# Kernel tuning notes

Measured on AMD Instinct MI355X. Metric: run time of the kernel, lower is better.

The kernel has to match this reference:

```python
import jax, jax.numpy as jnp
import numpy as np


def setup_inputs() -> dict:
    key = jax.random.key(0)
    ks = jax.random.split(key, 6)
    B, H, W, C = 4, 64, 64, 256
    D = 256  # d_model
    s = 0.02
    return {
        "features": jax.random.normal(ks[0], (B, H, W, C), dtype=jnp.float32),
        "Wq": jax.random.normal(ks[1], (C, D), dtype=jnp.float32) * s,
        "bq": jnp.zeros((D,), dtype=jnp.float32),
        "Wk": jax.random.normal(ks[2], (C, D), dtype=jnp.float32) * s,
        "bk": jnp.zeros((D,), dtype=jnp.float32),
        "Wv": jax.random.normal(ks[3], (C, D), dtype=jnp.float32) * s,
        "bv": jnp.zeros((D,), dtype=jnp.float32),
        "Wo": jax.random.normal(ks[4], (D, C), dtype=jnp.float32) * s,
        "bo": jnp.zeros((C,), dtype=jnp.float32),
    }


def reference(features, Wq, bq, Wk, bk, Wv, bv, Wo, bo):
    # features: [B, H, W, C] (NHWC). 1x1 convs are per-pixel GEMMs, so flatten
    # spatial dims to N = H*W tokens and do single-head self-attention.
    B, H, W, C = features.shape
    D = Wq.shape[1]
    x = features.reshape(B, H * W, C)          # [B, N, C]
    q = x @ Wq + bq                            # [B, N, D]
    k = x @ Wk + bk                            # [B, N, D]
    v = x @ Wv + bv                            # [B, N, D]
    scale = np.float32(1.0 / np.sqrt(D))
    scores = jnp.einsum("bnd,bmd->bnm", q, k) * scale   # [B, N, N]
    attn = jax.nn.softmax(scores, axis=-1)               # [B, N, N]
    out = jnp.einsum("bnm,bmd->bnd", attn, v)            # [B, N, D]
    out = out @ Wo + bo                                  # [B, N, C]
    return out.reshape(B, H, W, C)
```

## Files before the change

kernel.cpp:

```cpp
#include <hip/hip_runtime.h>
#include <hip/hip_bf16.h>


typedef __attribute__((ext_vector_type(8))) short short8;
typedef __attribute__((ext_vector_type(4))) short short4v;
typedef __attribute__((ext_vector_type(4))) float floatx4;

#define NB 4
#define NT 4096
#define CD 256
#define MTOT (NB * NT)

__device__ __forceinline__ short bf16s(float f) {
    union { float f; unsigned u; } a; a.f = f;
    unsigned u = a.u;
    return (short)((u + 0x7fffu + ((u >> 16) & 1u)) >> 16);
}

__device__ __forceinline__ float bf2f(short s) {
    union { unsigned u; float f; } a;
    a.u = ((unsigned)(unsigned short)s) << 16;
    return a.f;
}

__device__ __forceinline__ short8 ld8(const short* p) {
    return *(const short8*)p;
}

__device__ __forceinline__ floatx4 mfma16(short8 a, short8 b, floatx4 c) {
    return __builtin_amdgcn_mfma_f32_16x16x32_bf16(a, b, c, 0, 0, 0);
}

__device__ __forceinline__ void dma16(const void* g, void* l) {
    __builtin_amdgcn_global_load_lds(
        (const __attribute__((address_space(1))) void*)g,
        (__attribute__((address_space(3))) void*)l, 16, 0, 0);
}

__global__ __launch_bounds__(256) void k_convx(const float* __restrict__ x,
                                               short* __restrict__ xb) {
    int i = (blockIdx.x * 256 + threadIdx.x) * 4;
    float4 v = *(const float4*)(x + i);
    short4v o;
    o.x = bf16s(v.x); o.y = bf16s(v.y); o.z = bf16s(v.z); o.w = bf16s(v.w);
    *(short4v*)(xb + i) = o;
}

__global__ __launch_bounds__(256) void k_convw(const float* __restrict__ w0,
                                               const float* __restrict__ w1,
                                               const float* __restrict__ w2,
                                               const float* __restrict__ w3,
                                               short* __restrict__ wt) {
    int z = blockIdx.y;
    const float* w = (z == 0) ? w0 : (z == 1) ? w1 : (z == 2) ? w2 : w3;
    int c = blockIdx.x;
    int n = threadIdx.x;
    wt[z * 65536 + n * 256 + c] = bf16s(w[c * 256 + n]);
}

__global__ __launch_bounds__(256) void k_proj3(const short* __restrict__ A,
                                               const short* __restrict__ Wt,
                                               const float* __restrict__ bq,
                                               const float* __restrict__ bk,
                                               const float* __restrict__ bv,
                                               short* __restrict__ Qb,
                                               short* __restrict__ Kb,
                                               short* __restrict__ Vt) {
    __shared__ __align__(16) short Ws[16384];
    int z = blockIdx.z;
    const short* W = Wt + z * 65536;
    const float* bias = (z == 0) ? bq : (z == 1) ? bk : bv;
    float scale = (z == 0) ? 0.0625f : 1.0f;
    int m0 = blockIdx.x * 128;
    int n0 = blockIdx.y * 64;
    int tid = threadIdx.x;
    int w = tid >> 6, l = tid & 63, r = l & 15, q = l >> 4;

#pragma unroll
    for (int cg = 0; cg < 8; ++cg)
        dma16(W + (size_t)(n0 + w * 16 + r) * CD + (cg * 4 + q) * 8,
              &Ws[w * 4096 + cg * 512]);
    __syncthreads();

    const short* a0 = A + (size_t)(m0 + w * 32 + r) * CD;
    const short* a1 = a0 + 16 * CD;
    floatx4 acc[2][4];
#pragma unroll
    for (int rt = 0; rt < 2; ++rt)
#pragma unroll
        for (int j = 0; j < 4; ++j) acc[rt][j] = (floatx4){0.f, 0.f, 0.f, 0.f};
#pragma unroll
    for (int c = 0; c < 8; ++c) {
        short8 af0 = ld8(a0 + c * 32 + q * 8);
        short8 af1 = ld8(a1 + c * 32 + q * 8);
#pragma unroll
        for (int j = 0; j < 4; ++j) {
            short8 wf = ld8(&Ws[j * 4096 + c * 512 + l * 8]);
            acc[0][j] = mfma16(af0, wf, acc[0][j]);
            acc[1][j] = mfma16(af1, wf, acc[1][j]);
        }
    }
#pragma unroll
    for (int rt = 0; rt < 2; ++rt)
#pragma unroll
        for (int j = 0; j < 4; ++j) {
            int col = n0 + j * 16 + r;
            float bvv = bias[col];
#pragma unroll
            for (int i = 0; i < 4; ++i) {
                int row = m0 + w * 32 + rt * 16 + q * 4 + i;
                short s = bf16s((acc[rt][j][i] + bvv) * scale);
                if (z == 0) Qb[(size_t)row * CD + col] = s;
                else if (z == 1) Kb[(size_t)row * CD + col] = s;
                else {
                    int bb = row >> 12, lm = row & (NT - 1);
                    Vt[((size_t)bb * CD + col) * NT + lm] = s;
                }
            }
        }
}

__global__ __launch_bounds__(256, 3) void k_attn(const short* __restrict__ Qb,
                                                 const short* __restrict__ Kb,
                                                 const short* __restrict__ Vt,
                                                 short* __restrict__ Op0,
                                                 short* __restrict__ Op1,
                                                 short* __restrict__ Op2,
                                                 float* __restrict__ Lp,
                                                 int nks) {
    __shared__ __align__(16) short Ks[2][8192];
    __shared__ __align__(16) short P[64][36];

    const int tid = threadIdx.x;
    const int w = tid >> 6;
    const int l = tid & 63;
    const int r = l & 15, q = l >> 4;
    const int b = blockIdx.y;
    const int ks = blockIdx.z;
    const int m0 = blockIdx.x * 64;
    const int qq = 128 / nks, rem = 128 % nks;
    const int u0 = ks * qq + (ks < rem ? ks : rem);
    const int cnt = qq + (ks < rem ? 1 : 0);
    const int t0 = u0 * 32;
    const int tt_d = w & 1;
    const int cb_d = (w >> 1) * 4;
    const short* Qp = Qb + (size_t)b * NT * CD;
    const short* Kp = Kb + (size_t)b * NT * CD;
    const short* Vp = Vt + (size_t)b * CD * NT;
    short* Op = (ks == 0) ? Op0 : (ks == 1) ? Op1 : Op2;

    short8 qf[8];
#pragma unroll
    for (int c = 0; c < 8; ++c)
        qf[c] = ld8(Qp + (size_t)(m0 + w * 16 + r) * CD + c * 32 + q * 8);

    floatx4 o[4][4];
#pragma unroll
    for (int rt = 0; rt < 4; ++rt)
#pragma unroll
        for (int dt = 0; dt < 4; ++dt) o[rt][dt] = (floatx4){0.f, 0.f, 0.f, 0.f};
    float ls = 0.f;

#pragma unroll
    for (int j = 0; j < 4; ++j)
        dma16(Kp + (size_t)(t0 + tt_d * 16 + r) * CD + ((cb_d + j) * 4 + q) * 8,
              &Ks[0][tt_d * 4096 + (cb_d + j) * 512]);

#pragma unroll 1
    for (int it = 0; it < cnt; ++it) {
        const int p = it & 1;
        const int n0 = t0 + it * 32;
        __syncthreads();

        short8 vf[4];
#pragma unroll
        for (int dt = 0; dt < 4; ++dt)
            vf[dt] = ld8(Vp + (size_t)(w * 64 + dt * 16 + r) * NT + n0 + q * 8);

        if (it + 1 < cnt) {
#pragma unroll
            for (int j = 0; j < 4; ++j)
                dma16(Kp + (size_t)(n0 + 32 + tt_d * 16 + r) * CD + ((cb_d + j) * 4 + q) * 8,
                      &Ks[1 - p][tt_d * 4096 + (cb_d + j) * 512]);
        }

        floatx4 s0 = {0.f, 0.f, 0.f, 0.f};
        floatx4 s1 = {0.f, 0.f, 0.f, 0.f};
#pragma unroll
        for (int c = 0; c < 8; ++c) {
            s0 = mfma16(ld8(&Ks[p][c * 512 + l * 8]), qf[c], s0);
            s1 = mfma16(ld8(&Ks[p][4096 + c * 512 + l * 8]), qf[c], s1);
        }

#pragma unroll
        for (int tt = 0; tt < 2; ++tt) {
            floatx4 sv = tt ? s1 : s0;
            float e0 = __expf(sv[0]), e1 = __expf(sv[1]);
            float e2 = __expf(sv[2]), e3 = __expf(sv[3]);
            ls += (e0 + e1) + (e2 + e3);
            short4v pk;
            pk.x = bf16s(e0); pk.y = bf16s(e1); pk.z = bf16s(e2); pk.w = bf16s(e3);
            *(short4v*)&P[w * 16 + r][tt * 16 + q * 4] = pk;
        }
        asm volatile("s_waitcnt lgkmcnt(0)\n\ts_barrier" ::: "memory");

#pragma unroll
        for (int rt = 0; rt < 4; ++rt) {
            short8 pf = ld8(&P[rt * 16 + r][q * 8]);
#pragma unroll
            for (int dt = 0; dt < 4; ++dt)
                o[rt][dt] = mfma16(pf, vf[dt], o[rt][dt]);
        }
    }

    ls += __shfl_xor(ls, 16);
    ls += __shfl_xor(ls, 32);
    if (l < 16)
        Lp[(size_t)ks * MTOT + b * NT + m0 + w * 16 + l] = ls;

#pragma unroll
    for (int rt = 0; rt < 4; ++rt)
#pragma unroll
        for (int i = 0; i < 4; ++i) {
            int row = m0 + rt * 16 + q * 4 + i;
#pragma unroll
            for (int dt = 0; dt < 4; ++dt)
                Op[((size_t)b * NT + row) * CD + w * 64 + dt * 16 + r] =
                    bf16s(o[rt][dt][i]);
        }
}

__global__ __launch_bounds__(256) void k_oproj(const short* __restrict__ Op0,
                                               const short* __restrict__ Op1,
                                               const short* __restrict__ Op2,
                                               const float* __restrict__ Lp,
                                               const short* __restrict__ Wot,
                                               const float* __restrict__ bo,
                                               float* __restrict__ out, int nks) {
    __shared__ __align__(16) short Ws[16384];
    int m0 = blockIdx.x * 128;
    int n0 = blockIdx.y * 64;
    int tid = threadIdx.x;
    int w = tid >> 6, l = tid & 63, r = l & 15, q = l >> 4;

#pragma unroll
    for (int cg = 0; cg < 8; ++cg)
        dma16(Wot + (size_t)(n0 + w * 16 + r) * CD + (cg * 4 + q) * 8,
              &Ws[w * 4096 + cg * 512]);
    __syncthreads();

    int row0 = m0 + w * 32 + r;
    float lt0 = Lp[row0] + Lp[MTOT + row0];
    float lt1 = Lp[row0 + 16] + Lp[MTOT + row0 + 16];
    if (nks == 3) { lt0 += Lp[2 * MTOT + row0]; lt1 += Lp[2 * MTOT + row0 + 16]; }
    float inv0 = 1.0f / lt0, inv1 = 1.0f / lt1;
    const short* p00 = Op0 + (size_t)row0 * CD;
    const short* p01 = Op1 + (size_t)row0 * CD;
    const short* p02 = Op2 + (size_t)row0 * CD;
    floatx4 acc[2][4];
#pragma unroll
    for (int rt = 0; rt < 2; ++rt)
#pragma unroll
        for (int j = 0; j < 4; ++j) acc[rt][j] = (floatx4){0.f, 0.f, 0.f, 0.f};
#pragma unroll
    for (int c = 0; c < 8; ++c) {
        int off0 = c * 32 + q * 8, off1 = 16 * CD + c * 32 + q * 8;
        short8 x0 = ld8(p00 + off0), y0 = ld8(p01 + off0);
        short8 x1 = ld8(p00 + off1), y1 = ld8(p01 + off1);
        short8 af0, af1;
        if (nks == 3) {
            short8 z0 = ld8(p02 + off0), z1 = ld8(p02 + off1);
#pragma unroll
            for (int jj = 0; jj < 8; ++jj) {
                af0[jj] = bf16s((bf2f(x0[jj]) + bf2f(y0[jj]) + bf2f(z0[jj])) * inv0);
                af1[jj] = bf16s((bf2f(x1[jj]) + bf2f(y1[jj]) + bf2f(z1[jj])) * inv1);
            }
        } else {
#pragma unroll
            for (int jj = 0; jj < 8; ++jj) {
                af0[jj] = bf16s((bf2f(x0[jj]) + bf2f(y0[jj])) * inv0);
                af1[jj] = bf16s((bf2f(x1[jj]) + bf2f(y1[jj])) * inv1);
            }
        }
#pragma unroll
        for (int j = 0; j < 4; ++j) {
            short8 wf = ld8(&Ws[j * 4096 + c * 512 + l * 8]);
            acc[0][j] = mfma16(af0, wf, acc[0][j]);
            acc[1][j] = mfma16(af1, wf, acc[1][j]);
        }
    }
#pragma unroll
    for (int rt = 0; rt < 2; ++rt)
#pragma unroll
        for (int j = 0; j < 4; ++j) {
            int col = n0 + j * 16 + r;
            float bvv = bo[col];
#pragma unroll
            for (int i = 0; i < 4; ++i)
                out[(size_t)(m0 + w * 32 + rt * 16 + q * 4 + i) * CD + col] =
                    acc[rt][j][i] + bvv;
        }
}

extern "C" void kernel_launch(void* const* d_in, const int* in_sizes, int n_in,
                              void* d_out, int out_size, void* d_ws, size_t ws_size,
                              hipStream_t stream) {
    const float* x  = (const float*)d_in[0];
    const float* Wq = (const float*)d_in[1];
    const float* bq = (const float*)d_in[2];
    const float* Wk = (const float*)d_in[3];
    const float* bk = (const float*)d_in[4];
    const float* Wv = (const float*)d_in[5];
    const float* bv = (const float*)d_in[6];
    const float* Wo = (const float*)d_in[7];
    const float* bo = (const float*)d_in[8];
    float* out = (float*)d_out;

    char* ws = (char*)d_ws;
    const size_t MB = 1024u * 1024u;
    short* xb  = (short*)(ws);
    short* Op0 = (short*)(ws);
    short* Qb  = (short*)(ws + 8 * MB);
    short* Kb  = (short*)(ws + 16 * MB);
    short* Vt  = (short*)(ws + 24 * MB);
    short* Op1 = (short*)(ws + 32 * MB);
    short* Wt  = (short*)(ws + 40 * MB);
    float* Lp  = (float*)(ws + 40 * MB + 512 * 1024);
    short* Op2 = (short*)(ws + 41 * MB);

    int nks = (ws_size >= 49 * MB + 512 * 1024) ? 3 : 2;
    if (nks == 2) Op2 = Op1;

    k_convx<<<dim3(MTOT * CD / (256 * 4)), 256, 0, stream>>>(x, xb);
    k_convw<<<dim3(256, 4), 256, 0, stream>>>(Wq, Wk, Wv, Wo, Wt);
    k_proj3<<<dim3(MTOT / 128, CD / 64, 3), 256, 0, stream>>>(xb, Wt, bq, bk, bv, Qb, Kb, Vt);
    k_attn<<<dim3(NT / 64, NB, nks), 256, 0, stream>>>(Qb, Kb, Vt, Op0, Op1, Op2, Lp, nks);
    k_oproj<<<dim3(MTOT / 128, CD / 64), 256, 0, stream>>>(Op0, Op1, Op2, Lp, Wt + 196608, bo, out, nks);
}
```

Measured before the change: 258.7 us.

## Remap blocks to XCDs, allow 4-way KV split, packed bf16 convert

Flattens the grids of the projection, attention and output-projection kernels to 1D. Blocks are remapped so consecutive work items land on the same XCD (blk&7 interleave), which is meant to improve L2 locality for shared K/V and weight tiles. Adds a 4-way key split when the workspace is large enough, raises the attention occupancy hint to 4 blocks per CU, and replaces the manual bf16 rounding of the probabilities with the v_cvt_pk_bf16_f32 instruction. The extra split adds another partial-output buffer and more reduction traffic in the output projection, and the higher occupancy hint may cause register spills.

```diff
diff --git a/kernel.cpp b/kernel.cpp
--- a/kernel.cpp
+++ b/kernel.cpp
@@ -67,12 +67,15 @@
                                                short* __restrict__ Kb,
                                                short* __restrict__ Vt) {
     __shared__ __align__(16) short Ws[16384];
-    int z = blockIdx.z;
+    int blk = blockIdx.x;
+    int wk = (blk & 7) * 192 + (blk >> 3);
+    int m = wk / 12, rest = wk - m * 12;
+    int z = rest >> 2, y = rest & 3;
     const short* W = Wt + z * 65536;
     const float* bias = (z == 0) ? bq : (z == 1) ? bk : bv;
     float scale = (z == 0) ? 0.0625f : 1.0f;
-    int m0 = blockIdx.x * 128;
-    int n0 = blockIdx.y * 64;
+    int m0 = m * 128;
+    int n0 = y * 64;
     int tid = threadIdx.x;
     int w = tid >> 6, l = tid & 63, r = l & 15, q = l >> 4;
 
@@ -120,12 +123,13 @@
         }
 }
 
-__global__ __launch_bounds__(256, 3) void k_attn(const short* __restrict__ Qb,
+__global__ __launch_bounds__(256, 4) void k_attn(const short* __restrict__ Qb,
                                                  const short* __restrict__ Kb,
                                                  const short* __restrict__ Vt,
                                                  short* __restrict__ Op0,
                                                  short* __restrict__ Op1,
                                                  short* __restrict__ Op2,
+                                                 short* __restrict__ Op3,
                                                  float* __restrict__ Lp,
                                                  int nks) {
     __shared__ __align__(16) short Ks[2][8192];
@@ -135,9 +139,14 @@
     const int w = tid >> 6;
     const int l = tid & 63;
     const int r = l & 15, q = l >> 4;
-    const int b = blockIdx.y;
-    const int ks = blockIdx.z;
-    const int m0 = blockIdx.x * 64;
+    const int nbk = gridDim.x;
+    const int blk = blockIdx.x;
+    const int wk = (blk & 7) * (nbk >> 3) + (blk >> 3);
+    const int bx = wk & 63;
+    const int co = wk >> 6;
+    const int b = co / nks;
+    const int ks = co - b * nks;
+    const int m0 = bx * 64;
     const int qq = 128 / nks, rem = 128 % nks;
     const int u0 = ks * qq + (ks < rem ? ks : rem);
     const int cnt = qq + (ks < rem ? 1 : 0);
@@ -147,7 +156,7 @@
     const short* Qp = Qb + (size_t)b * NT * CD;
     const short* Kp = Kb + (size_t)b * NT * CD;
     const short* Vp = Vt + (size_t)b * CD * NT;
-    short* Op = (ks == 0) ? Op0 : (ks == 1) ? Op1 : Op2;
+    short* Op = (ks == 0) ? Op0 : (ks == 1) ? Op1 : (ks == 2) ? Op2 : Op3;
 
     short8 qf[8];
 #pragma unroll
@@ -198,9 +207,11 @@
             float e0 = __expf(sv[0]), e1 = __expf(sv[1]);
             float e2 = __expf(sv[2]), e3 = __expf(sv[3]);
             ls += (e0 + e1) + (e2 + e3);
-            short4v pk;
-            pk.x = bf16s(e0); pk.y = bf16s(e1); pk.z = bf16s(e2); pk.w = bf16s(e3);
-            *(short4v*)&P[w * 16 + r][tt * 16 + q * 4] = pk;
+            unsigned pk01, pk23;
+            asm("v_cvt_pk_bf16_f32 %0, %1, %2" : "=v"(pk01) : "v"(e0), "v"(e1));
+            asm("v_cvt_pk_bf16_f32 %0, %1, %2" : "=v"(pk23) : "v"(e2), "v"(e3));
+            uint2 pk; pk.x = pk01; pk.y = pk23;
+            *(uint2*)&P[w * 16 + r][tt * 16 + q * 4] = pk;
         }
         asm volatile("s_waitcnt lgkmcnt(0)\n\ts_barrier" ::: "memory");
 
@@ -233,13 +244,16 @@
 __global__ __launch_bounds__(256) void k_oproj(const short* __restrict__ Op0,
                                                const short* __restrict__ Op1,
                                                const short* __restrict__ Op2,
+                                               const short* __restrict__ Op3,
                                                const float* __restrict__ Lp,
                                                const short* __restrict__ Wot,
                                                const float* __restrict__ bo,
                                                float* __restrict__ out, int nks) {
     __shared__ __align__(16) short Ws[16384];
-    int m0 = blockIdx.x * 128;
-    int n0 = blockIdx.y * 64;
+    int blk = blockIdx.x;
+    int wk = (blk & 7) * 64 + (blk >> 3);
+    int m0 = (wk >> 2) * 128;
+    int n0 = (wk & 3) * 64;
     int tid = threadIdx.x;
     int w = tid >> 6, l = tid & 63, r = l & 15, q = l >> 4;
 
@@ -252,11 +266,13 @@
     int row0 = m0 + w * 32 + r;
     float lt0 = Lp[row0] + Lp[MTOT + row0];
     float lt1 = Lp[row0 + 16] + Lp[MTOT + row0 + 16];
-    if (nks == 3) { lt0 += Lp[2 * MTOT + row0]; lt1 += Lp[2 * MTOT + row0 + 16]; }
+    if (nks >= 3) { lt0 += Lp[2 * (size_t)MTOT + row0]; lt1 += Lp[2 * (size_t)MTOT + row0 + 16]; }
+    if (nks >= 4) { lt0 += Lp[3 * (size_t)MTOT + row0]; lt1 += Lp[3 * (size_t)MTOT + row0 + 16]; }
     float inv0 = 1.0f / lt0, inv1 = 1.0f / lt1;
-    const short* p00 = Op0 + (size_t)row0 * CD;
-    const short* p01 = Op1 + (size_t)row0 * CD;
-    const short* p02 = Op2 + (size_t)row0 * CD;
+    const short* p0 = Op0 + (size_t)row0 * CD;
+    const short* p1 = Op1 + (size_t)row0 * CD;
+    const short* p2 = Op2 + (size_t)row0 * CD;
+    const short* p3 = Op3 + (size_t)row0 * CD;
     floatx4 acc[2][4];
 #pragma unroll
     for (int rt = 0; rt < 2; ++rt)
@@ -265,22 +281,35 @@
 #pragma unroll
     for (int c = 0; c < 8; ++c) {
         int off0 = c * 32 + q * 8, off1 = 16 * CD + c * 32 + q * 8;
-        short8 x0 = ld8(p00 + off0), y0 = ld8(p01 + off0);
-        short8 x1 = ld8(p00 + off1), y1 = ld8(p01 + off1);
+        short8 x0 = ld8(p0 + off0), y0 = ld8(p1 + off0);
+        short8 x1 = ld8(p0 + off1), y1 = ld8(p1 + off1);
+        float f0[8], f1[8];
+#pragma unroll
+        for (int jj = 0; jj < 8; ++jj) {
+            f0[jj] = bf2f(x0[jj]) + bf2f(y0[jj]);
+            f1[jj] = bf2f(x1[jj]) + bf2f(y1[jj]);
+        }
+        if (nks >= 3) {
+            short8 z0 = ld8(p2 + off0), z1 = ld8(p2 + off1);
+#pragma unroll
+            for (int jj = 0; jj < 8; ++jj) {
+                f0[jj] += bf2f(z0[jj]);
+                f1[jj] += bf2f(z1[jj]);
+            }
+        }
+        if (nks >= 4) {
+            short8 u0 = ld8(p3 + off0), u1 = ld8(p3 + off1);
+#pragma unroll
+            for (int jj = 0; jj < 8; ++jj) {
+                f0[jj] += bf2f(u0[jj]);
+                f1[jj] += bf2f(u1[jj]);
+            }
+        }
         short8 af0, af1;
-        if (nks == 3) {
-            short8 z0 = ld8(p02 + off0), z1 = ld8(p02 + off1);
-#pragma unroll
-            for (int jj = 0; jj < 8; ++jj) {
-                af0[jj] = bf16s((bf2f(x0[jj]) + bf2f(y0[jj]) + bf2f(z0[jj])) * inv0);
-                af1[jj] = bf16s((bf2f(x1[jj]) + bf2f(y1[jj]) + bf2f(z1[jj])) * inv1);
-            }
-        } else {
-#pragma unroll
-            for (int jj = 0; jj < 8; ++jj) {
-                af0[jj] = bf16s((bf2f(x0[jj]) + bf2f(y0[jj])) * inv0);
-                af1[jj] = bf16s((bf2f(x1[jj]) + bf2f(y1[jj])) * inv1);
-            }
+#pragma unroll
+        for (int jj = 0; jj < 8; ++jj) {
+            af0[jj] = bf16s(f0[jj] * inv0);
+            af1[jj] = bf16s(f1[jj] * inv1);
         }
 #pragma unroll
         for (int j = 0; j < 4; ++j) {
@@ -326,14 +355,15 @@
     short* Op1 = (short*)(ws + 32 * MB);
     short* Wt  = (short*)(ws + 40 * MB);
     float* Lp  = (float*)(ws + 40 * MB + 512 * 1024);
-    short* Op2 = (short*)(ws + 41 * MB);
-
-    int nks = (ws_size >= 49 * MB + 512 * 1024) ? 3 : 2;
-    if (nks == 2) Op2 = Op1;
+
+    int nks = (ws_size >= 57 * MB) ? 4
+            : (ws_size >= 49 * MB + 512 * 1024) ? 3 : 2;
+    short* Op2 = (nks >= 3) ? (short*)(ws + 41 * MB) : Op1;
+    short* Op3 = (nks >= 4) ? (short*)(ws + 49 * MB) : Op1;
 
     k_convx<<<dim3(MTOT * CD / (256 * 4)), 256, 0, stream>>>(x, xb);
     k_convw<<<dim3(256, 4), 256, 0, stream>>>(Wq, Wk, Wv, Wo, Wt);
-    k_proj3<<<dim3(MTOT / 128, CD / 64, 3), 256, 0, stream>>>(xb, Wt, bq, bk, bv, Qb, Kb, Vt);
-    k_attn<<<dim3(NT / 64, NB, nks), 256, 0, stream>>>(Qb, Kb, Vt, Op0, Op1, Op2, Lp, nks);
-    k_oproj<<<dim3(MTOT / 128, CD / 64), 256, 0, stream>>>(Op0, Op1, Op2, Lp, Wt + 196608, bo, out, nks);
-}
+    k_proj3<<<dim3(1536), 256, 0, stream>>>(xb, Wt, bq, bk, bv, Qb, Kb, Vt);
+    k_attn<<<dim3(64 * NB * nks), 256, 0, stream>>>(Qb, Kb, Vt, Op0, Op1, Op2, Op3, Lp, nks);
+    k_oproj<<<dim3(512), 256, 0, stream>>>(Op0, Op1, Op2, Op3, Lp, Wt + 196608, bo, out, nks);
+}
```

Result: slower. 341.2 us (+31.9%).
